# Kernel tuning notes

Hardware: AMD Instinct MI355X
Metric: run time of the kernel (lower is better)

The kernel has to match this reference:

```python
import jax, jax.numpy as jnp
import numpy as np

DIM = 512
NUM_HEADS = 8


def setup_inputs() -> dict:
    key = jax.random.key(0)
    ks = jax.random.split(key, 9)
    B, C, H, W = 8, DIM, 32, 32
    s = 1.0 / np.sqrt(DIM)  # conv-style init scale
    return {
        "x": jax.random.normal(ks[0], (B, C, H, W), jnp.float32),
        "Wq": jax.random.normal(ks[1], (DIM, DIM), jnp.float32) * s,
        "bq": jnp.zeros((DIM,), jnp.float32),
        "Wk": jax.random.normal(ks[2], (DIM, DIM), jnp.float32) * s,
        "bk": jnp.zeros((DIM,), jnp.float32),
        "Wv": jax.random.normal(ks[3], (DIM, DIM), jnp.float32) * s,
        "bv": jnp.zeros((DIM,), jnp.float32),
        "Wo": jax.random.normal(ks[4], (DIM, DIM), jnp.float32) * s,
        "bo": jnp.zeros((DIM,), jnp.float32),
    }


def _proj(x, W, b):
    # 1x1 conv == per-pixel linear over channels: [out_c, in_c] x [b, in_c, h, w]
    return jnp.einsum('oc,bchw->bohw', W, x) + b[None, :, None, None]


def reference(x, Wq, bq, Wk, bk, Wv, bv, Wo, bo):
    b, c, h, w = x.shape
    g = NUM_HEADS
    dh = c // g  # per-head channels
    q = _proj(x, Wq, bq)
    k = _proj(x, Wk, bk)
    v = _proj(x, Wv, bv)
    # 'b (g c) h w -> (b g) c (h w)'
    def split_heads(t):
        return t.reshape(b, g, dh, h * w).reshape(b * g, dh, h * w)
    q, k, v = split_heads(q), split_heads(k), split_heads(v)
    # note: scale uses full dim (as in the source), not per-head dim
    a = jnp.einsum('bcs,bct->bst', q, k) / jnp.sqrt(jnp.float32(c))
    a = jax.nn.softmax(a, axis=-1)  # dropout is identity at inference
    o = jnp.einsum('bst,bct->bcs', a, v)  # [(b g), dh, s]
    o = o.reshape(b, g * dh, h, w)  # '(b g) c (h w) -> b (g c) h w'
    return x + _proj(o, Wo, bo)
```

## Files before the change

### kernel.cpp

```cpp
#include <hip/hip_runtime.h>

typedef unsigned short u16;
typedef __attribute__((ext_vector_type(8))) short short8;
typedef __attribute__((ext_vector_type(4))) short sh4;
typedef __attribute__((ext_vector_type(2))) int int2v;
typedef __attribute__((ext_vector_type(4))) float floatx4;

__device__ __forceinline__ float b2f(u16 u) {
  unsigned int x = ((unsigned int)u) << 16;
  return __builtin_bit_cast(float, x);
}
__device__ __forceinline__ u16 f2b(float f) {
  unsigned int x = __builtin_bit_cast(unsigned int, f);
  unsigned int r = (x + 0x7FFFu + ((x >> 16) & 1u)) >> 16;
  return (u16)r;
}
__device__ __forceinline__ unsigned int pk2bf(float a, float b) {
  unsigned int ua = __builtin_bit_cast(unsigned int, a) + 0x8000u;
  unsigned int ub = __builtin_bit_cast(unsigned int, b) + 0x8000u;
  return __builtin_amdgcn_perm(ub, ua, 0x07060302u);
}

#if __has_builtin(__builtin_amdgcn_mfma_f32_16x16x16bf16_1k)
#define MFMA16(a, b, c) __builtin_amdgcn_mfma_f32_16x16x16bf16_1k((a), (b), (c), 0, 0, 0)
#define MFMA16_DRAIN()
#else
__device__ __forceinline__ floatx4 mfma16_fb(sh4 a, sh4 b, floatx4 c) {
  asm volatile("s_nop 1\n\tv_mfma_f32_16x16x16_bf16 %0, %1, %2, %0"
               : "+v"(c) : "v"(a), "v"(b));
  return c;
}
#define MFMA16(a, b, c) mfma16_fb((a), (b), (c))
#define MFMA16_DRAIN() asm volatile("s_nop 7\n\ts_nop 7\n\ts_nop 7")
#endif

#if __has_builtin(__builtin_amdgcn_exp2f)
#define EXP2F(x) __builtin_amdgcn_exp2f(x)
#else
#define EXP2F(x) __expf((x) * 0.6931471805599453f)
#endif

#define MFMA32(a, b, c) __builtin_amdgcn_mfma_f32_16x16x32_bf16((a), (b), (c), 0, 0, 0)

#define GLL16(g, l) __builtin_amdgcn_global_load_lds(                         \
    (const __attribute__((address_space(1))) unsigned int*)(g),               \
    (__attribute__((address_space(3))) unsigned int*)(l), 16, 0, 0)

#define SC_LOG2E 0.06375872f

__device__ __forceinline__ int detect_fp32(const u16* __restrict__ x) {
  __shared__ int cnt;
  if (threadIdx.x == 0) cnt = 0;
  __syncthreads();
  int c = 0;
  if (threadIdx.x < 256) {
#pragma unroll
    for (int i = 0; i < 16; ++i) {
      u16 u = x[threadIdx.x * 16 + i];
      if (((u >> 7) & 0xFF) >= 0xC8) c++;
    }
  }
  if (c) atomicAdd(&cnt, c);
  __syncthreads();
  return cnt > 32;
}

__global__ __launch_bounds__(256) void prep(
    const u16* __restrict__ x,
    const u16* w0, const u16* w1, const u16* w2, const u16* w3,
    const u16* c0, const u16* c1, const u16* c2, const u16* c3,
    u16* __restrict__ xT, u16* __restrict__ Wc, u16* __restrict__ bc, int b0) {
  const int fp32 = detect_fp32(x);
  const int tid = threadIdx.x;
  if (blockIdx.y < 8) {
    __shared__ u16 t[64][65];
    const int lb = blockIdx.z, b = b0 + lb;
    const int p0 = blockIdx.x * 64, cc0 = blockIdx.y * 64;
    const int tx = tid & 63, ty = tid >> 6;
    if (fp32) {
      const float* xb = (const float*)x + (long)b * 524288;
#pragma unroll
      for (int i = 0; i < 16; ++i) {
        int c = ty + i * 4;
        t[c][tx] = f2b(xb[(long)(cc0 + c) * 1024 + p0 + tx]);
      }
    } else {
      const u16* xb = x + (long)b * 524288;
#pragma unroll
      for (int i = 0; i < 16; ++i) {
        int c = ty + i * 4;
        t[c][tx] = xb[(long)(cc0 + c) * 1024 + p0 + tx];
      }
    }
    __syncthreads();
    u16* xTb = xT + (long)lb * 524288;
#pragma unroll
    for (int i = 0; i < 16; ++i) {
      int p = ty + i * 4;
      xTb[(long)(p0 + p) * 512 + cc0 + tx] = t[tx][p];
    }
  } else {
    const u16* srcs[8] = {w0, w1, w2, w3, c0, c1, c2, c3};
    const int nthreads = gridDim.z * 16 * 256;
    const int flat = (blockIdx.z * 16 + blockIdx.x) * 256 + tid;
    for (int vi = flat; vi < 131072; vi += nthreads) {
      int w = vi >> 15;
      int off = (vi & 32767) * 8;
      u16* dst = Wc + w * 262144 + off;
      if (fp32) {
        const float* s = (const float*)srcs[w] + off;
        u16 tmp[8];
#pragma unroll
        for (int r = 0; r < 8; ++r) tmp[r] = f2b(s[r]);
        *(int4*)dst = *(const int4*)tmp;
      } else {
        *(int4*)dst = *(const int4*)(srcs[w] + off);
      }
    }
    for (int gi = flat; gi < 2048; gi += nthreads) {
      int t2 = gi >> 9;
      bc[gi] = fp32 ? f2b(((const float*)srcs[4 + t2])[gi & 511]) : srcs[4 + t2][gi & 511];
    }
  }
}

struct GemmLds64 {
  u16 As0[128][32], As1[128][32];
  u16 Bs0[128][32], Bs1[128][32];
};

__device__ __forceinline__ void gemm_core64(const u16* __restrict__ A, int lda,
                                            const u16* __restrict__ B, int ldb,
                                            int m0, int n0, int K,
                                            GemmLds64& lds, floatx4 (&acc)[4][4]) {
  const int tid = threadIdx.x;
  const int wave = tid >> 6, lane = tid & 63;
  const int quad = lane >> 4, l15 = lane & 15;
  const int wm = (wave >> 1) * 64, wn = (wave & 1) * 64;
  const int lrow = lane >> 2, lcol = (lane & 3) * 8;
  for (int k0 = 0; k0 < K; k0 += 64) {
    __syncthreads();
#pragma unroll
    for (int it = 0; it < 2; ++it) {
      const int rbase = wave * 32 + it * 16;
      const u16* Ar = A + (long)(m0 + rbase + lrow) * lda + k0 + lcol;
      GLL16(Ar, &lds.As0[rbase][0]);
      GLL16(Ar + 32, &lds.As1[rbase][0]);
      const u16* Br = B + (long)(n0 + rbase + lrow) * ldb + k0 + lcol;
      GLL16(Br, &lds.Bs0[rbase][0]);
      GLL16(Br + 32, &lds.Bs1[rbase][0]);
    }
    __syncthreads();
    short8 af[4], bf[4];
#pragma unroll
    for (int i = 0; i < 4; ++i)
      af[i] = *(const short8*)&lds.As0[wm + i * 16 + l15][quad * 8];
#pragma unroll
    for (int j = 0; j < 4; ++j)
      bf[j] = *(const short8*)&lds.Bs0[wn + j * 16 + l15][quad * 8];
#pragma unroll
    for (int i = 0; i < 4; ++i)
#pragma unroll
      for (int j = 0; j < 4; ++j)
        acc[i][j] = MFMA32(af[i], bf[j], acc[i][j]);
#pragma unroll
    for (int i = 0; i < 4; ++i)
      af[i] = *(const short8*)&lds.As1[wm + i * 16 + l15][quad * 8];
#pragma unroll
    for (int j = 0; j < 4; ++j)
      bf[j] = *(const short8*)&lds.Bs1[wn + j * 16 + l15][quad * 8];
#pragma unroll
    for (int i = 0; i < 4; ++i)
#pragma unroll
      for (int j = 0; j < 4; ++j)
        acc[i][j] = MFMA32(af[i], bf[j], acc[i][j]);
  }
}

__global__ __launch_bounds__(256) void gemm_qkv(
    const u16* __restrict__ xT, const u16* __restrict__ Wc,
    const u16* __restrict__ bc, u16* __restrict__ Qt, u16* __restrict__ Kt,
    u16* __restrict__ Vv) {
  __shared__ GemmLds64 lds;
  const long bz = blockIdx.x;
  const u16* xb = xT + bz * 524288;
  const int bx = blockIdx.y;
  const int qk = bx < 64;
  const int t = qk ? bx : bx - 64;
  const int m0 = (t >> 3) * 128, n0 = (t & 7) * 128;
  const u16* A = qk ? xb : (Wc + 524288);
  const u16* B = qk ? Wc : xb;
  floatx4 acc[4][4] = {};
  gemm_core64(A, 512, B, 512, m0, n0, 512, lds, acc);
  const int lane = threadIdx.x & 63, wave = threadIdx.x >> 6;
  const int quad = lane >> 4, l15 = lane & 15;
  const int wm = (wave >> 1) * 64, wn = (wave & 1) * 64;
  if (qk) {
    u16* Qz = Qt + bz * 524288;
    u16* Kz = Kt + bz * 524288;
#pragma unroll
    for (int i = 0; i < 4; ++i)
#pragma unroll
      for (int j = 0; j < 4; ++j)
#pragma unroll
        for (int r = 0; r < 4; ++r) {
          int gm = m0 + wm + i * 16 + quad * 4 + r;
          int gn = n0 + wn + j * 16 + l15;
          float v = acc[i][j][r] + b2f(bc[gn]);
          if (gn < 512) Qz[(long)gm * 512 + gn] = f2b(v * SC_LOG2E);
          else Kz[(long)gm * 512 + gn - 512] = f2b(v);
        }
  } else {
    u16* Vz = Vv + bz * 524288;
    const u16* bv = bc + 1024;
#pragma unroll
    for (int i = 0; i < 4; ++i)
#pragma unroll
      for (int j = 0; j < 4; ++j)
#pragma unroll
        for (int r = 0; r < 4; ++r) {
          int gm = m0 + wm + i * 16 + quad * 4 + r;
          int gn = n0 + wn + j * 16 + l15;
          float v = acc[i][j][r] + b2f(bv[gm]);
          Vz[(long)gm * 1024 + gn] = f2b(v);
        }
  }
}

struct OutLds64 {
  u16 As0[128][32], As1[128][32];
  u16 Bs0[64][32], Bs1[64][32];
};

__global__ __launch_bounds__(256) void gemm_out(
    const u16* __restrict__ Wo, const u16* __restrict__ bo,
    const u16* __restrict__ Ow, const u16* __restrict__ xraw,
    u16* __restrict__ out) {
  const int fp32 = detect_fp32(xraw);
  __shared__ OutLds64 lds;
  const long bz = blockIdx.x;
  const u16* B = Ow + bz * 524288;
  const int m0 = blockIdx.z * 128, n0 = blockIdx.y * 64;
  const int tid = threadIdx.x;
  const int wave = tid >> 6, lane = tid & 63;
  const int quad = lane >> 4, l15 = lane & 15;
  const int lrow = lane >> 2, lcol = (lane & 3) * 8;

  floatx4 acc[2][4] = {};

  for (int k0 = 0; k0 < 512; k0 += 64) {
    __syncthreads();
    {
      const int ra = wave * 32;
      const u16* A0 = Wo + (long)(m0 + ra + lrow) * 512 + k0 + lcol;
      const u16* A1 = Wo + (long)(m0 + ra + 16 + lrow) * 512 + k0 + lcol;
      GLL16(A0, &lds.As0[ra][0]);
      GLL16(A0 + 32, &lds.As1[ra][0]);
      GLL16(A1, &lds.As0[ra + 16][0]);
      GLL16(A1 + 32, &lds.As1[ra + 16][0]);
      const u16* Br = B + (long)(n0 + wave * 16 + lrow) * 512 + k0 + lcol;
      GLL16(Br, &lds.Bs0[wave * 16][0]);
      GLL16(Br + 32, &lds.Bs1[wave * 16][0]);
    }
    __syncthreads();
#pragma unroll
    for (int i = 0; i < 2; ++i) {
      short8 af = *(const short8*)&lds.As0[wave * 32 + i * 16 + l15][quad * 8];
#pragma unroll
      for (int j = 0; j < 4; ++j) {
        short8 bf = *(const short8*)&lds.Bs0[j * 16 + l15][quad * 8];
        acc[i][j] = MFMA32(af, bf, acc[i][j]);
      }
    }
#pragma unroll
    for (int i = 0; i < 2; ++i) {
      short8 af = *(const short8*)&lds.As1[wave * 32 + i * 16 + l15][quad * 8];
#pragma unroll
      for (int j = 0; j < 4; ++j) {
        short8 bf = *(const short8*)&lds.Bs1[j * 16 + l15][quad * 8];
        acc[i][j] = MFMA32(af, bf, acc[i][j]);
      }
    }
  }

#pragma unroll
  for (int i = 0; i < 2; ++i)
#pragma unroll
    for (int j = 0; j < 4; ++j)
#pragma unroll
      for (int r = 0; r < 4; ++r) {
        int gm = m0 + wave * 32 + i * 16 + quad * 4 + r;
        int gn = n0 + j * 16 + l15;
        float v = acc[i][j][r] + b2f(bo[gm]);
        long idx = bz * 524288 + (long)gm * 1024 + gn;
        if (fp32) {
          v += ((const float*)xraw)[idx];
          ((float*)out)[idx] = v;
        } else {
          v += b2f(xraw[idx]);
          out[idx] = f2b(v);
        }
      }
}

#define AP 72
__global__ __launch_bounds__(256, 2) void attn(
    const u16* __restrict__ Qt, const u16* __restrict__ Kt,
    const u16* __restrict__ V, u16* __restrict__ O) {
  __shared__ alignas(16) u16 Ks[2][64][AP];
  __shared__ alignas(16) u16 Vs[2][64][AP];
  const int bg = blockIdx.x;
  const int lb = bg >> 3, head = bg & 7;
  const int s0 = blockIdx.y * 128;
  const int tid = threadIdx.x;
  const int wave = tid >> 6, lane = tid & 63;
  const int quad = lane >> 4, l15 = lane & 15;

  const u16* Qb = Qt + (long)lb * 524288 + head * 64;
  const u16* Kb = Kt + (long)lb * 524288 + head * 64;
  const u16* Vb = V + (long)(lb * 512 + head * 64) * 1024;
  u16* Ob = O + (long)lb * 524288 + head * 64;

  short8 bq[2][2];
#pragma unroll
  for (int qb = 0; qb < 2; ++qb)
#pragma unroll
    for (int kk = 0; kk < 2; ++kk)
      bq[qb][kk] = *(const short8*)&Qb[(long)(s0 + wave * 32 + qb * 16 + l15) * 512 +
                                       kk * 32 + quad * 8];

  const int r0 = tid >> 3, o0 = (tid & 7) * 8;
  int4 kreg0, kreg1, vreg0, vreg1;
  kreg0 = *(const int4*)&Kb[(long)r0 * 512 + o0];
  kreg1 = *(const int4*)&Kb[(long)(r0 + 32) * 512 + o0];
  vreg0 = *(const int4*)&Vb[(long)r0 * 1024 + o0];
  vreg1 = *(const int4*)&Vb[(long)(r0 + 32) * 1024 + o0];
  *(int4*)&Ks[0][r0][o0] = kreg0;
  *(int4*)&Ks[0][r0 + 32][o0] = kreg1;
  *(int4*)&Vs[0][r0][o0] = vreg0;
  *(int4*)&Vs[0][r0 + 32][o0] = vreg1;

  floatx4 acc[2][4] = {};
  floatx4 accl[2] = {};
  const sh4 ones = {(short)0x3F80, (short)0x3F80, (short)0x3F80, (short)0x3F80};

  for (int it16 = 0; it16 < 16; ++it16) {
    const int buf = it16 & 1;
    const int t0n = (it16 + 1) * 64;
    if (it16 < 15) {
      kreg0 = *(const int4*)&Kb[(long)(t0n + r0) * 512 + o0];
      kreg1 = *(const int4*)&Kb[(long)(t0n + r0 + 32) * 512 + o0];
      vreg0 = *(const int4*)&Vb[(long)r0 * 1024 + t0n + o0];
      vreg1 = *(const int4*)&Vb[(long)(r0 + 32) * 1024 + t0n + o0];
    }
    __syncthreads();

    floatx4 p[2][4] = {};
#pragma unroll
    for (int kk = 0; kk < 2; ++kk) {
      short8 ak[4];
#pragma unroll
      for (int mi = 0; mi < 4; ++mi)
        ak[mi] = *(const short8*)&Ks[buf][mi * 16 + l15][kk * 32 + quad * 8];
#pragma unroll
      for (int qb = 0; qb < 2; ++qb)
#pragma unroll
        for (int mi = 0; mi < 4; ++mi)
          p[qb][mi] = MFMA32(ak[mi], bq[qb][kk], p[qb][mi]);
    }

    sh4 pk[2][4];
#pragma unroll
    for (int qb = 0; qb < 2; ++qb)
#pragma unroll
      for (int mi = 0; mi < 4; ++mi) {
        float e0 = EXP2F(p[qb][mi][0]);
        float e1 = EXP2F(p[qb][mi][1]);
        float e2 = EXP2F(p[qb][mi][2]);
        float e3 = EXP2F(p[qb][mi][3]);
        int2v w;
        w.x = (int)pk2bf(e0, e1);
        w.y = (int)pk2bf(e2, e3);
        pk[qb][mi] = __builtin_bit_cast(sh4, w);
      }

#pragma unroll
    for (int qb = 0; qb < 2; ++qb)
#pragma unroll
      for (int mi = 0; mi < 4; ++mi) accl[qb] = MFMA16(ones, pk[qb][mi], accl[qb]);

#pragma unroll
    for (int mi = 0; mi < 4; ++mi) {
      sh4 av[4];
#pragma unroll
      for (int ci = 0; ci < 4; ++ci)
        av[ci] = *(const sh4*)&Vs[buf][ci * 16 + l15][mi * 16 + quad * 4];
#pragma unroll
      for (int qb = 0; qb < 2; ++qb)
#pragma unroll
        for (int ci = 0; ci < 4; ++ci)
          acc[qb][ci] = MFMA16(av[ci], pk[qb][mi], acc[qb][ci]);
    }

    if (it16 < 15) {
      const int nb = 1 - buf;
      *(int4*)&Ks[nb][r0][o0] = kreg0;
      *(int4*)&Ks[nb][r0 + 32][o0] = kreg1;
      *(int4*)&Vs[nb][r0][o0] = vreg0;
      *(int4*)&Vs[nb][r0 + 32][o0] = vreg1;
    }
  }
  MFMA16_DRAIN();

  const float inv0 = 1.0f / accl[0][0];
  const float inv1 = 1.0f / accl[1][0];

  u16 (*Os)[AP] = (u16(*)[AP]) & Ks[0][0][0];
  __syncthreads();
#pragma unroll
  for (int qb = 0; qb < 2; ++qb) {
    const float inv = qb ? inv1 : inv0;
#pragma unroll
    for (int ci = 0; ci < 4; ++ci) {
      int2v w;
      w.x = (int)pk2bf(acc[qb][ci][0] * inv, acc[qb][ci][1] * inv);
      w.y = (int)pk2bf(acc[qb][ci][2] * inv, acc[qb][ci][3] * inv);
      *(int2v*)&Os[wave * 32 + qb * 16 + l15][ci * 16 + quad * 4] = w;
    }
  }
  __syncthreads();
  {
    const int srow = tid >> 1, cb = (tid & 1) * 32;
#pragma unroll
    for (int c = 0; c < 32; c += 8)
      *(int4*)&Ob[(long)(s0 + srow) * 512 + cb + c] = *(const int4*)&Os[srow][cb + c];
  }
}

extern "C" void kernel_launch(void* const* d_in, const int* in_sizes, int n_in,
                              void* d_out, int out_size, void* d_ws, size_t ws_size,
                              hipStream_t stream) {
  const u16* x  = (const u16*)d_in[0];
  const u16* Wq = (const u16*)d_in[1];
  const u16* bq = (const u16*)d_in[2];
  const u16* Wk = (const u16*)d_in[3];
  const u16* bk = (const u16*)d_in[4];
  const u16* Wv = (const u16*)d_in[5];
  const u16* bv = (const u16*)d_in[6];
  const u16* Wo = (const u16*)d_in[7];
  const u16* bo = (const u16*)d_in[8];
  u16* out = (u16*)d_out;
  u16* ws = (u16*)d_ws;

  const size_t PLAN_A_BYTES = 27267072;

  if (ws_size >= PLAN_A_BYTES) {
    u16* xT = ws;
    u16* Kt = ws + 4194304;
    u16* Vv = ws + 8388608;
    u16* Wc = ws + 12582912;
    u16* bc = ws + 13631488;
    u16* Qt = out;
    u16* Ow = xT;

    prep<<<dim3(16, 9, 8), 256, 0, stream>>>(x, Wq, Wk, Wv, Wo,
                                             bq, bk, bv, bo, xT, Wc, bc, 0);
    gemm_qkv<<<dim3(8, 96), 256, 0, stream>>>(xT, Wc, bc, Qt, Kt, Vv);
    attn<<<dim3(64, 8), 256, 0, stream>>>(Qt, Kt, Vv, Ow);
    gemm_out<<<dim3(8, 16, 4), 256, 0, stream>>>(Wc + 786432, bc + 1536, Ow, x, out);
  } else {
    u16* Ow = ws;
    u16* Kt = ws + 4194304;
    u16* Vv = ws + 6291456;
    u16* Wc = ws + 8388608;
    u16* bc = ws + 9437184;
    u16* Qt = out;

    for (int phase = 0; phase < 2; ++phase) {
      const int b0 = phase * 4;
      u16* xT = Ow + (long)phase * 2097152;
      prep<<<dim3(16, 9, 4), 256, 0, stream>>>(x, Wq, Wk, Wv, Wo,
                                               bq, bk, bv, bo, xT, Wc, bc, b0);
      gemm_qkv<<<dim3(4, 96), 256, 0, stream>>>(xT, Wc, bc, Qt, Kt, Vv);
      attn<<<dim3(32, 8), 256, 0, stream>>>(Qt, Kt, Vv, Ow + (long)b0 * 524288);
    }
    gemm_out<<<dim3(8, 16, 4), 256, 0, stream>>>(Wc + 786432, bc + 1536, Ow, x, out);
  }
}
```

Baseline: 161.1 us.

## Fuse input transpose and weight conversion into QKV GEMM, drop prep kernel

Removes the separate prep kernel that transposed x to bf16 and converted the weights. The QKV GEMM now reads x (fp32 or bf16) directly, converts and transposes it while staging into LDS, and converts the weights on the fly. gemm_out converts Wo on the fly in the same way. This saves one launch and a full round trip of x through the workspace. The cost is an fp32 staging path that uses scalar LDS stores with bank conflicts and recomputes conversions in every tile, instead of async global-to-LDS loads.

```diff
diff --git a/kernel.cpp b/kernel.cpp
--- a/kernel.cpp
+++ b/kernel.cpp
@@ -65,90 +65,118 @@
   return cnt > 32;
 }
 
-__global__ __launch_bounds__(256) void prep(
-    const u16* __restrict__ x,
-    const u16* w0, const u16* w1, const u16* w2, const u16* w3,
-    const u16* c0, const u16* c1, const u16* c2, const u16* c3,
-    u16* __restrict__ xT, u16* __restrict__ Wc, u16* __restrict__ bc, int b0) {
-  const int fp32 = detect_fp32(x);
-  const int tid = threadIdx.x;
-  if (blockIdx.y < 8) {
-    __shared__ u16 t[64][65];
-    const int lb = blockIdx.z, b = b0 + lb;
-    const int p0 = blockIdx.x * 64, cc0 = blockIdx.y * 64;
-    const int tx = tid & 63, ty = tid >> 6;
-    if (fp32) {
-      const float* xb = (const float*)x + (long)b * 524288;
-#pragma unroll
-      for (int i = 0; i < 16; ++i) {
-        int c = ty + i * 4;
-        t[c][tx] = f2b(xb[(long)(cc0 + c) * 1024 + p0 + tx]);
-      }
-    } else {
-      const u16* xb = x + (long)b * 524288;
-#pragma unroll
-      for (int i = 0; i < 16; ++i) {
-        int c = ty + i * 4;
-        t[c][tx] = xb[(long)(cc0 + c) * 1024 + p0 + tx];
-      }
-    }
-    __syncthreads();
-    u16* xTb = xT + (long)lb * 524288;
-#pragma unroll
-    for (int i = 0; i < 16; ++i) {
-      int p = ty + i * 4;
-      xTb[(long)(p0 + p) * 512 + cc0 + tx] = t[tx][p];
-    }
-  } else {
-    const u16* srcs[8] = {w0, w1, w2, w3, c0, c1, c2, c3};
-    const int nthreads = gridDim.z * 16 * 256;
-    const int flat = (blockIdx.z * 16 + blockIdx.x) * 256 + tid;
-    for (int vi = flat; vi < 131072; vi += nthreads) {
-      int w = vi >> 15;
-      int off = (vi & 32767) * 8;
-      u16* dst = Wc + w * 262144 + off;
-      if (fp32) {
-        const float* s = (const float*)srcs[w] + off;
-        u16 tmp[8];
-#pragma unroll
-        for (int r = 0; r < 8; ++r) tmp[r] = f2b(s[r]);
-        *(int4*)dst = *(const int4*)tmp;
-      } else {
-        *(int4*)dst = *(const int4*)(srcs[w] + off);
-      }
-    }
-    for (int gi = flat; gi < 2048; gi += nthreads) {
-      int t2 = gi >> 9;
-      bc[gi] = fp32 ? f2b(((const float*)srcs[4 + t2])[gi & 511]) : srcs[4 + t2][gi & 511];
-    }
-  }
+__device__ __forceinline__ float bload(const u16* p, long i, int fp32) {
+  return fp32 ? ((const float*)p)[i] : b2f(p[i]);
 }
 
 struct GemmLds64 {
   u16 As0[128][32], As1[128][32];
   u16 Bs0[128][32], Bs1[128][32];
 };
-
-__device__ __forceinline__ void gemm_core64(const u16* __restrict__ A, int lda,
-                                            const u16* __restrict__ B, int ldb,
-                                            int m0, int n0, int K,
-                                            GemmLds64& lds, floatx4 (&acc)[4][4]) {
+struct OutLds64 {
+  u16 As0[128][32], As1[128][32];
+  u16 Bs0[64][32], Bs1[64][32];
+};
+#define AP 72
+struct AttnLds {
+  alignas(16) u16 Ks[2][64][AP];
+  alignas(16) u16 Vs[2][64][AP];
+};
+
+__device__ __forceinline__ void stage_xT(const u16* __restrict__ x, int b,
+                                         int fp32, int row0, int k0,
+                                         u16 (*__restrict__ S0)[32],
+                                         u16 (*__restrict__ S1)[32]) {
+  const int tid = threadIdx.x;
+  const int cl = tid & 63, pc = tid >> 6;
+  u16(*__restrict__ S)[32] = (cl < 32) ? S0 : S1;
+  const int c31 = cl & 31;
+  if (fp32) {
+    const float* src = (const float*)x + (long)b * 524288 +
+                       (long)(k0 + cl) * 1024 + row0 + pc * 32;
+#pragma unroll
+    for (int q = 0; q < 4; ++q) {
+      float4 f0 = *(const float4*)(src + q * 8);
+      float4 f1 = *(const float4*)(src + q * 8 + 4);
+      u16 tmp[8] = {f2b(f0.x), f2b(f0.y), f2b(f0.z), f2b(f0.w),
+                    f2b(f1.x), f2b(f1.y), f2b(f1.z), f2b(f1.w)};
+#pragma unroll
+      for (int e = 0; e < 8; ++e) S[pc * 32 + q * 8 + e][c31] = tmp[e];
+    }
+  } else {
+    const u16* src = x + (long)b * 524288 + (long)(k0 + cl) * 1024 + row0 + pc * 32;
+#pragma unroll
+    for (int q = 0; q < 4; ++q) {
+      int4 v = *(const int4*)(src + q * 8);
+      const u16* t = (const u16*)&v;
+#pragma unroll
+      for (int e = 0; e < 8; ++e) S[pc * 32 + q * 8 + e][c31] = t[e];
+    }
+  }
+}
+
+__device__ __forceinline__ void stage_w(const u16* __restrict__ W, int fp32,
+                                        int row0, int ld, int k0,
+                                        u16 (*__restrict__ S0)[32],
+                                        u16 (*__restrict__ S1)[32], int rbase_w) {
+  const int lane = threadIdx.x & 63;
+  const int lrow = lane >> 2, lcol = (lane & 3) * 8;
+  if (!fp32) {
+#pragma unroll
+    for (int it = 0; it < 2; ++it) {
+      const int rb = rbase_w + it * 16;
+      const u16* Wr = W + (long)(row0 + rb + lrow) * ld + k0 + lcol;
+      GLL16(Wr, &S0[rb][0]);
+      GLL16(Wr + 32, &S1[rb][0]);
+    }
+  } else {
+#pragma unroll
+    for (int it = 0; it < 2; ++it) {
+      const int rb = rbase_w + it * 16;
+      const float* Wr = (const float*)W + (long)(row0 + rb + lrow) * ld + k0 + lcol;
+      u16 a[8], b[8];
+#pragma unroll
+      for (int e = 0; e < 8; ++e) {
+        a[e] = f2b(Wr[e]);
+        b[e] = f2b(Wr[32 + e]);
+      }
+      *(int4*)&S0[rb + lrow][lcol] = *(const int4*)a;
+      *(int4*)&S1[rb + lrow][lcol] = *(const int4*)b;
+    }
+  }
+}
+
+__global__ __launch_bounds__(256) void gemm_qkvT(
+    const u16* __restrict__ x, const u16* __restrict__ Wq,
+    const u16* __restrict__ Wk, const u16* __restrict__ Wv,
+    const u16* __restrict__ bq, const u16* __restrict__ bk,
+    const u16* __restrict__ bv, u16* Qt, u16* __restrict__ Kt,
+    u16* __restrict__ Vv, int b0) {
+  const int fp32 = detect_fp32(x);
+  __shared__ GemmLds64 lds;
+  const long bz = blockIdx.x;
+  const int b = b0 + (int)bz;
+  const int bx = blockIdx.y;
+  const int qk = bx < 64;
+  const int t = qk ? bx : bx - 64;
+  const int m0 = (t >> 3) * 128, n0 = (t & 7) * 128;
+  const u16* Wsel = qk ? (n0 < 512 ? Wq : Wk) : Wv;
+  const int wrow0 = qk ? (n0 & 511) : m0;
+
   const int tid = threadIdx.x;
   const int wave = tid >> 6, lane = tid & 63;
   const int quad = lane >> 4, l15 = lane & 15;
   const int wm = (wave >> 1) * 64, wn = (wave & 1) * 64;
-  const int lrow = lane >> 2, lcol = (lane & 3) * 8;
-  for (int k0 = 0; k0 < K; k0 += 64) {
+
+  floatx4 acc[4][4] = {};
+  for (int k0 = 0; k0 < 512; k0 += 64) {
     __syncthreads();
-#pragma unroll
-    for (int it = 0; it < 2; ++it) {
-      const int rbase = wave * 32 + it * 16;
-      const u16* Ar = A + (long)(m0 + rbase + lrow) * lda + k0 + lcol;
-      GLL16(Ar, &lds.As0[rbase][0]);
-      GLL16(Ar + 32, &lds.As1[rbase][0]);
-      const u16* Br = B + (long)(n0 + rbase + lrow) * ldb + k0 + lcol;
-      GLL16(Br, &lds.Bs0[rbase][0]);
-      GLL16(Br + 32, &lds.Bs1[rbase][0]);
+    if (qk) {
+      stage_xT(x, b, fp32, m0, k0, lds.As0, lds.As1);
+      stage_w(Wsel, fp32, wrow0, 512, k0, lds.Bs0, lds.Bs1, wave * 32);
+    } else {
+      stage_w(Wsel, fp32, wrow0, 512, k0, lds.As0, lds.As1, wave * 32);
+      stage_xT(x, b, fp32, n0, k0, lds.Bs0, lds.Bs1);
     }
     __syncthreads();
     short8 af[4], bf[4];
@@ -175,26 +203,7 @@
       for (int j = 0; j < 4; ++j)
         acc[i][j] = MFMA32(af[i], bf[j], acc[i][j]);
   }
-}
-
-__global__ __launch_bounds__(256) void gemm_qkv(
-    const u16* __restrict__ xT, const u16* __restrict__ Wc,
-    const u16* __restrict__ bc, u16* __restrict__ Qt, u16* __restrict__ Kt,
-    u16* __restrict__ Vv) {
-  __shared__ GemmLds64 lds;
-  const long bz = blockIdx.x;
-  const u16* xb = xT + bz * 524288;
-  const int bx = blockIdx.y;
-  const int qk = bx < 64;
-  const int t = qk ? bx : bx - 64;
-  const int m0 = (t >> 3) * 128, n0 = (t & 7) * 128;
-  const u16* A = qk ? xb : (Wc + 524288);
-  const u16* B = qk ? Wc : xb;
-  floatx4 acc[4][4] = {};
-  gemm_core64(A, 512, B, 512, m0, n0, 512, lds, acc);
-  const int lane = threadIdx.x & 63, wave = threadIdx.x >> 6;
-  const int quad = lane >> 4, l15 = lane & 15;
-  const int wm = (wave >> 1) * 64, wn = (wave & 1) * 64;
+
   if (qk) {
     u16* Qz = Qt + bz * 524288;
     u16* Kz = Kt + bz * 524288;
@@ -206,13 +215,12 @@
         for (int r = 0; r < 4; ++r) {
           int gm = m0 + wm + i * 16 + quad * 4 + r;
           int gn = n0 + wn + j * 16 + l15;
-          float v = acc[i][j][r] + b2f(bc[gn]);
+          float v = acc[i][j][r] + bload(gn < 512 ? bq : bk, gn & 511, fp32);
           if (gn < 512) Qz[(long)gm * 512 + gn] = f2b(v * SC_LOG2E);
           else Kz[(long)gm * 512 + gn - 512] = f2b(v);
         }
   } else {
     u16* Vz = Vv + bz * 524288;
-    const u16* bv = bc + 1024;
 #pragma unroll
     for (int i = 0; i < 4; ++i)
 #pragma unroll
@@ -221,16 +229,143 @@
         for (int r = 0; r < 4; ++r) {
           int gm = m0 + wm + i * 16 + quad * 4 + r;
           int gn = n0 + wn + j * 16 + l15;
-          float v = acc[i][j][r] + b2f(bv[gm]);
+          float v = acc[i][j][r] + bload(bv, gm, fp32);
           Vz[(long)gm * 1024 + gn] = f2b(v);
         }
   }
 }
 
-struct OutLds64 {
-  u16 As0[128][32], As1[128][32];
-  u16 Bs0[64][32], Bs1[64][32];
-};
+__global__ __launch_bounds__(256, 2) void attn(
+    const u16* __restrict__ Qt, const u16* __restrict__ Kt,
+    const u16* __restrict__ V, u16* __restrict__ O) {
+  __shared__ AttnLds L;
+  const int bg = blockIdx.x;
+  const int lb = bg >> 3, head = bg & 7;
+  const int s0 = blockIdx.y * 128;
+  const int tid = threadIdx.x;
+  const int wave = tid >> 6, lane = tid & 63;
+  const int quad = lane >> 4, l15 = lane & 15;
+
+  const u16* Qb = Qt + (long)lb * 524288 + head * 64;
+  const u16* Kb = Kt + (long)lb * 524288 + head * 64;
+  const u16* Vb = V + (long)(lb * 512 + head * 64) * 1024;
+  u16* Ob = O + (long)lb * 524288 + head * 64;
+
+  short8 bq[2][2];
+#pragma unroll
+  for (int qb = 0; qb < 2; ++qb)
+#pragma unroll
+    for (int kk = 0; kk < 2; ++kk)
+      bq[qb][kk] = *(const short8*)&Qb[(long)(s0 + wave * 32 + qb * 16 + l15) * 512 +
+                                       kk * 32 + quad * 8];
+
+  const int r0 = tid >> 3, o0 = (tid & 7) * 8;
+  int4 kreg0, kreg1, vreg0, vreg1;
+  kreg0 = *(const int4*)&Kb[(long)r0 * 512 + o0];
+  kreg1 = *(const int4*)&Kb[(long)(r0 + 32) * 512 + o0];
+  vreg0 = *(const int4*)&Vb[(long)r0 * 1024 + o0];
+  vreg1 = *(const int4*)&Vb[(long)(r0 + 32) * 1024 + o0];
+  *(int4*)&L.Ks[0][r0][o0] = kreg0;
+  *(int4*)&L.Ks[0][r0 + 32][o0] = kreg1;
+  *(int4*)&L.Vs[0][r0][o0] = vreg0;
+  *(int4*)&L.Vs[0][r0 + 32][o0] = vreg1;
+
+  floatx4 acc[2][4] = {};
+  floatx4 accl[2] = {};
+  const sh4 ones = {(short)0x3F80, (short)0x3F80, (short)0x3F80, (short)0x3F80};
+
+  for (int it16 = 0; it16 < 16; ++it16) {
+    const int buf = it16 & 1;
+    const int t0n = (it16 + 1) * 64;
+    if (it16 < 15) {
+      kreg0 = *(const int4*)&Kb[(long)(t0n + r0) * 512 + o0];
+      kreg1 = *(const int4*)&Kb[(long)(t0n + r0 + 32) * 512 + o0];
+      vreg0 = *(const int4*)&Vb[(long)r0 * 1024 + t0n + o0];
+      vreg1 = *(const int4*)&Vb[(long)(r0 + 32) * 1024 + t0n + o0];
+    }
+    __syncthreads();
+
+    floatx4 p[2][4] = {};
+#pragma unroll
+    for (int kk = 0; kk < 2; ++kk) {
+      short8 ak[4];
+#pragma unroll
+      for (int mi = 0; mi < 4; ++mi)
+        ak[mi] = *(const short8*)&L.Ks[buf][mi * 16 + l15][kk * 32 + quad * 8];
+#pragma unroll
+      for (int qb = 0; qb < 2; ++qb)
+#pragma unroll
+        for (int mi = 0; mi < 4; ++mi)
+          p[qb][mi] = MFMA32(ak[mi], bq[qb][kk], p[qb][mi]);
+    }
+
+    sh4 pk[2][4];
+#pragma unroll
+    for (int qb = 0; qb < 2; ++qb)
+#pragma unroll
+      for (int mi = 0; mi < 4; ++mi) {
+        float e0 = EXP2F(p[qb][mi][0]);
+        float e1 = EXP2F(p[qb][mi][1]);
+        float e2 = EXP2F(p[qb][mi][2]);
+        float e3 = EXP2F(p[qb][mi][3]);
+        int2v w;
+        w.x = (int)pk2bf(e0, e1);
+        w.y = (int)pk2bf(e2, e3);
+        pk[qb][mi] = __builtin_bit_cast(sh4, w);
+      }
+
+#pragma unroll
+    for (int qb = 0; qb < 2; ++qb)
+#pragma unroll
+      for (int mi = 0; mi < 4; ++mi) accl[qb] = MFMA16(ones, pk[qb][mi], accl[qb]);
+
+#pragma unroll
+    for (int mi = 0; mi < 4; ++mi) {
+      sh4 av[4];
+#pragma unroll
+      for (int ci = 0; ci < 4; ++ci)
+        av[ci] = *(const sh4*)&L.Vs[buf][ci * 16 + l15][mi * 16 + quad * 4];
+#pragma unroll
+      for (int qb = 0; qb < 2; ++qb)
+#pragma unroll
+        for (int ci = 0; ci < 4; ++ci)
+          acc[qb][ci] = MFMA16(av[ci], pk[qb][mi], acc[qb][ci]);
+    }
+
+    if (it16 < 15) {
+      const int nb = 1 - buf;
+      *(int4*)&L.Ks[nb][r0][o0] = kreg0;
+      *(int4*)&L.Ks[nb][r0 + 32][o0] = kreg1;
+      *(int4*)&L.Vs[nb][r0][o0] = vreg0;
+      *(int4*)&L.Vs[nb][r0 + 32][o0] = vreg1;
+    }
+  }
+  MFMA16_DRAIN();
+
+  const float inv0 = 1.0f / accl[0][0];
+  const float inv1 = 1.0f / accl[1][0];
+
+  u16 (*Os)[AP] = (u16(*)[AP]) & L.Ks[0][0][0];
+  __syncthreads();
+#pragma unroll
+  for (int qb = 0; qb < 2; ++qb) {
+    const float inv = qb ? inv1 : inv0;
+#pragma unroll
+    for (int ci = 0; ci < 4; ++ci) {
+      int2v w;
+      w.x = (int)pk2bf(acc[qb][ci][0] * inv, acc[qb][ci][1] * inv);
+      w.y = (int)pk2bf(acc[qb][ci][2] * inv, acc[qb][ci][3] * inv);
+      *(int2v*)&Os[wave * 32 + qb * 16 + l15][ci * 16 + quad * 4] = w;
+    }
+  }
+  __syncthreads();
+  {
+    const int srow = tid >> 1, cb = (tid & 1) * 32;
+#pragma unroll
+    for (int c = 0; c < 32; c += 8)
+      *(int4*)&Ob[(long)(s0 + srow) * 512 + cb + c] = *(const int4*)&Os[srow][cb + c];
+  }
+}
 
 __global__ __launch_bounds__(256) void gemm_out(
     const u16* __restrict__ Wo, const u16* __restrict__ bo,
@@ -250,14 +385,8 @@
 
   for (int k0 = 0; k0 < 512; k0 += 64) {
     __syncthreads();
+    stage_w(Wo, fp32, m0, 512, k0, lds.As0, lds.As1, wave * 32);
     {
-      const int ra = wave * 32;
-      const u16* A0 = Wo + (long)(m0 + ra + lrow) * 512 + k0 + lcol;
-      const u16* A1 = Wo + (long)(m0 + ra + 16 + lrow) * 512 + k0 + lcol;
-      GLL16(A0, &lds.As0[ra][0]);
-      GLL16(A0 + 32, &lds.As1[ra][0]);
-      GLL16(A1, &lds.As0[ra + 16][0]);
-      GLL16(A1 + 32, &lds.As1[ra + 16][0]);
       const u16* Br = B + (long)(n0 + wave * 16 + lrow) * 512 + k0 + lcol;
       GLL16(Br, &lds.Bs0[wave * 16][0]);
       GLL16(Br + 32, &lds.Bs1[wave * 16][0]);
@@ -291,7 +420,7 @@
       for (int r = 0; r < 4; ++r) {
         int gm = m0 + wave * 32 + i * 16 + quad * 4 + r;
         int gn = n0 + j * 16 + l15;
-        float v = acc[i][j][r] + b2f(bo[gm]);
+        float v = acc[i][j][r] + bload(bo, gm, fp32);
         long idx = bz * 524288 + (long)gm * 1024 + gn;
         if (fp32) {
           v += ((const float*)xraw)[idx];
@@ -301,140 +430,6 @@
           out[idx] = f2b(v);
         }
       }
-}
-
-#define AP 72
-__global__ __launch_bounds__(256, 2) void attn(
-    const u16* __restrict__ Qt, const u16* __restrict__ Kt,
-    const u16* __restrict__ V, u16* __restrict__ O) {
-  __shared__ alignas(16) u16 Ks[2][64][AP];
-  __shared__ alignas(16) u16 Vs[2][64][AP];
-  const int bg = blockIdx.x;
-  const int lb = bg >> 3, head = bg & 7;
-  const int s0 = blockIdx.y * 128;
-  const int tid = threadIdx.x;
-  const int wave = tid >> 6, lane = tid & 63;
-  const int quad = lane >> 4, l15 = lane & 15;
-
-  const u16* Qb = Qt + (long)lb * 524288 + head * 64;
-  const u16* Kb = Kt + (long)lb * 524288 + head * 64;
-  const u16* Vb = V + (long)(lb * 512 + head * 64) * 1024;
-  u16* Ob = O + (long)lb * 524288 + head * 64;
-
-  short8 bq[2][2];
-#pragma unroll
-  for (int qb = 0; qb < 2; ++qb)
-#pragma unroll
-    for (int kk = 0; kk < 2; ++kk)
-      bq[qb][kk] = *(const short8*)&Qb[(long)(s0 + wave * 32 + qb * 16 + l15) * 512 +
-                                       kk * 32 + quad * 8];
-
-  const int r0 = tid >> 3, o0 = (tid & 7) * 8;
-  int4 kreg0, kreg1, vreg0, vreg1;
-  kreg0 = *(const int4*)&Kb[(long)r0 * 512 + o0];
-  kreg1 = *(const int4*)&Kb[(long)(r0 + 32) * 512 + o0];
-  vreg0 = *(const int4*)&Vb[(long)r0 * 1024 + o0];
-  vreg1 = *(const int4*)&Vb[(long)(r0 + 32) * 1024 + o0];
-  *(int4*)&Ks[0][r0][o0] = kreg0;
-  *(int4*)&Ks[0][r0 + 32][o0] = kreg1;
-  *(int4*)&Vs[0][r0][o0] = vreg0;
-  *(int4*)&Vs[0][r0 + 32][o0] = vreg1;
-
-  floatx4 acc[2][4] = {};
-  floatx4 accl[2] = {};
-  const sh4 ones = {(short)0x3F80, (short)0x3F80, (short)0x3F80, (short)0x3F80};
-
-  for (int it16 = 0; it16 < 16; ++it16) {
-    const int buf = it16 & 1;
-    const int t0n = (it16 + 1) * 64;
-    if (it16 < 15) {
-      kreg0 = *(const int4*)&Kb[(long)(t0n + r0) * 512 + o0];
-      kreg1 = *(const int4*)&Kb[(long)(t0n + r0 + 32) * 512 + o0];
-      vreg0 = *(const int4*)&Vb[(long)r0 * 1024 + t0n + o0];
-      vreg1 = *(const int4*)&Vb[(long)(r0 + 32) * 1024 + t0n + o0];
-    }
-    __syncthreads();
-
-    floatx4 p[2][4] = {};
-#pragma unroll
-    for (int kk = 0; kk < 2; ++kk) {
-      short8 ak[4];
-#pragma unroll
-      for (int mi = 0; mi < 4; ++mi)
-        ak[mi] = *(const short8*)&Ks[buf][mi * 16 + l15][kk * 32 + quad * 8];
-#pragma unroll
-      for (int qb = 0; qb < 2; ++qb)
-#pragma unroll
-        for (int mi = 0; mi < 4; ++mi)
-          p[qb][mi] = MFMA32(ak[mi], bq[qb][kk], p[qb][mi]);
-    }
-
-    sh4 pk[2][4];
-#pragma unroll
-    for (int qb = 0; qb < 2; ++qb)
-#pragma unroll
-      for (int mi = 0; mi < 4; ++mi) {
-        float e0 = EXP2F(p[qb][mi][0]);
-        float e1 = EXP2F(p[qb][mi][1]);
-        float e2 = EXP2F(p[qb][mi][2]);
-        float e3 = EXP2F(p[qb][mi][3]);
-        int2v w;
-        w.x = (int)pk2bf(e0, e1);
-        w.y = (int)pk2bf(e2, e3);
-        pk[qb][mi] = __builtin_bit_cast(sh4, w);
-      }
-
-#pragma unroll
-    for (int qb = 0; qb < 2; ++qb)
-#pragma unroll
-      for (int mi = 0; mi < 4; ++mi) accl[qb] = MFMA16(ones, pk[qb][mi], accl[qb]);
-
-#pragma unroll
-    for (int mi = 0; mi < 4; ++mi) {
-      sh4 av[4];
-#pragma unroll
-      for (int ci = 0; ci < 4; ++ci)
-        av[ci] = *(const sh4*)&Vs[buf][ci * 16 + l15][mi * 16 + quad * 4];
-#pragma unroll
-      for (int qb = 0; qb < 2; ++qb)
-#pragma unroll
-        for (int ci = 0; ci < 4; ++ci)
-          acc[qb][ci] = MFMA16(av[ci], pk[qb][mi], acc[qb][ci]);
-    }
-
-    if (it16 < 15) {
-      const int nb = 1 - buf;
-      *(int4*)&Ks[nb][r0][o0] = kreg0;
-      *(int4*)&Ks[nb][r0 + 32][o0] = kreg1;
-      *(int4*)&Vs[nb][r0][o0] = vreg0;
-      *(int4*)&Vs[nb][r0 + 32][o0] = vreg1;
-    }
-  }
-  MFMA16_DRAIN();
-
-  const float inv0 = 1.0f / accl[0][0];
-  const float inv1 = 1.0f / accl[1][0];
-
-  u16 (*Os)[AP] = (u16(*)[AP]) & Ks[0][0][0];
-  __syncthreads();
-#pragma unroll
-  for (int qb = 0; qb < 2; ++qb) {
-    const float inv = qb ? inv1 : inv0;
-#pragma unroll
-    for (int ci = 0; ci < 4; ++ci) {
-      int2v w;
-      w.x = (int)pk2bf(acc[qb][ci][0] * inv, acc[qb][ci][1] * inv);
-      w.y = (int)pk2bf(acc[qb][ci][2] * inv, acc[qb][ci][3] * inv);
-      *(int2v*)&Os[wave * 32 + qb * 16 + l15][ci * 16 + quad * 4] = w;
-    }
-  }
-  __syncthreads();
-  {
-    const int srow = tid >> 1, cb = (tid & 1) * 32;
-#pragma unroll
-    for (int c = 0; c < 32; c += 8)
-      *(int4*)&Ob[(long)(s0 + srow) * 512 + cb + c] = *(const int4*)&Os[srow][cb + c];
-  }
 }
 
 extern "C" void kernel_launch(void* const* d_in, const int* in_sizes, int n_in,
@@ -452,38 +447,30 @@
   u16* out = (u16*)d_out;
   u16* ws = (u16*)d_ws;
 
-  const size_t PLAN_A_BYTES = 27267072;
+  const size_t PLAN_A_BYTES = 25165824;
 
   if (ws_size >= PLAN_A_BYTES) {
-    u16* xT = ws;
-    u16* Kt = ws + 4194304;
-    u16* Vv = ws + 8388608;
-    u16* Wc = ws + 12582912;
-    u16* bc = ws + 13631488;
+    u16* Kt = ws;
+    u16* Vv = ws + 4194304;
+    u16* Ow = ws + 8388608;
     u16* Qt = out;
-    u16* Ow = xT;
-
-    prep<<<dim3(16, 9, 8), 256, 0, stream>>>(x, Wq, Wk, Wv, Wo,
-                                             bq, bk, bv, bo, xT, Wc, bc, 0);
-    gemm_qkv<<<dim3(8, 96), 256, 0, stream>>>(xT, Wc, bc, Qt, Kt, Vv);
+
+    gemm_qkvT<<<dim3(8, 96), 256, 0, stream>>>(x, Wq, Wk, Wv, bq, bk, bv,
+                                               Qt, Kt, Vv, 0);
     attn<<<dim3(64, 8), 256, 0, stream>>>(Qt, Kt, Vv, Ow);
-    gemm_out<<<dim3(8, 16, 4), 256, 0, stream>>>(Wc + 786432, bc + 1536, Ow, x, out);
+    gemm_out<<<dim3(8, 16, 4), 256, 0, stream>>>(Wo, bo, Ow, x, out);
   } else {
     u16* Ow = ws;
     u16* Kt = ws + 4194304;
     u16* Vv = ws + 6291456;
-    u16* Wc = ws + 8388608;
-    u16* bc = ws + 9437184;
     u16* Qt = out;
 
     for (int phase = 0; phase < 2; ++phase) {
       const int b0 = phase * 4;
-      u16* xT = Ow + (long)phase * 2097152;
-      prep<<<dim3(16, 9, 4), 256, 0, stream>>>(x, Wq, Wk, Wv, Wo,
-                                               bq, bk, bv, bo, xT, Wc, bc, b0);
-      gemm_qkv<<<dim3(4, 96), 256, 0, stream>>>(xT, Wc, bc, Qt, Kt, Vv);
+      gemm_qkvT<<<dim3(4, 96), 256, 0, stream>>>(x, Wq, Wk, Wv, bq, bk, bv,
+                                                 Qt, Kt, Vv, b0);
       attn<<<dim3(32, 8), 256, 0, stream>>>(Qt, Kt, Vv, Ow + (long)b0 * 524288);
     }
-    gemm_out<<<dim3(8, 16, 4), 256, 0, stream>>>(Wc + 786432, bc + 1536, Ow, x, out);
-  }
-}
+    gemm_out<<<dim3(8, 16, 4), 256, 0, stream>>>(Wo, bo, Ow, x, out);
+  }
+}
```

Measured after the change: 206.9 us. 28.5% more time.

## Double-buffer LDS tiles in QKV and output GEMMs to overlap loads with MFMA

Applied to the files above, without the earlier changes.

Both projection GEMMs move from a load-sync-compute loop over K-steps of 64 to a two-buffer ping-pong over K-steps of 32. The next tile's global-to-LDS load is issued before the MFMAs on the current buffer, and one barrier per step replaces two. The aim is to hide global load latency behind matrix math. The cost is twice as many loop iterations and barriers, with less compute per step to cover each load.

```diff
diff --git a/kernel.cpp b/kernel.cpp
--- a/kernel.cpp
+++ b/kernel.cpp
@@ -124,56 +124,52 @@
   }
 }
 
-struct GemmLds64 {
-  u16 As0[128][32], As1[128][32];
-  u16 Bs0[128][32], Bs1[128][32];
+struct GemmLdsP {
+  u16 As[2][128][32], Bs[2][128][32];
 };
 
-__device__ __forceinline__ void gemm_core64(const u16* __restrict__ A, int lda,
-                                            const u16* __restrict__ B, int ldb,
-                                            int m0, int n0, int K,
-                                            GemmLds64& lds, floatx4 (&acc)[4][4]) {
+__device__ __forceinline__ void gemm_stage(const u16* __restrict__ A, int lda,
+                                           const u16* __restrict__ B, int ldb,
+                                           int m0, int n0, int k0, int buf,
+                                           GemmLdsP& lds) {
+  const int tid = threadIdx.x;
+  const int wave = tid >> 6, lane = tid & 63;
+  const int lrow = lane >> 2, lcol = (lane & 3) * 8;
+#pragma unroll
+  for (int it = 0; it < 2; ++it) {
+    const int rbase = wave * 32 + it * 16;
+    GLL16(A + (long)(m0 + rbase + lrow) * lda + k0 + lcol, &lds.As[buf][rbase][0]);
+    GLL16(B + (long)(n0 + rbase + lrow) * ldb + k0 + lcol, &lds.Bs[buf][rbase][0]);
+  }
+}
+
+__device__ __forceinline__ void gemm_core_pipe(const u16* __restrict__ A, int lda,
+                                               const u16* __restrict__ B, int ldb,
+                                               int m0, int n0, int K,
+                                               GemmLdsP& lds, floatx4 (&acc)[4][4]) {
   const int tid = threadIdx.x;
   const int wave = tid >> 6, lane = tid & 63;
   const int quad = lane >> 4, l15 = lane & 15;
   const int wm = (wave >> 1) * 64, wn = (wave & 1) * 64;
-  const int lrow = lane >> 2, lcol = (lane & 3) * 8;
-  for (int k0 = 0; k0 < K; k0 += 64) {
-    __syncthreads();
-#pragma unroll
-    for (int it = 0; it < 2; ++it) {
-      const int rbase = wave * 32 + it * 16;
-      const u16* Ar = A + (long)(m0 + rbase + lrow) * lda + k0 + lcol;
-      GLL16(Ar, &lds.As0[rbase][0]);
-      GLL16(Ar + 32, &lds.As1[rbase][0]);
-      const u16* Br = B + (long)(n0 + rbase + lrow) * ldb + k0 + lcol;
-      GLL16(Br, &lds.Bs0[rbase][0]);
-      GLL16(Br + 32, &lds.Bs1[rbase][0]);
-    }
-    __syncthreads();
+
+  gemm_stage(A, lda, B, ldb, m0, n0, 0, 0, lds);
+  __syncthreads();
+  for (int k0 = 0; k0 < K; k0 += 32) {
+    const int buf = (k0 >> 5) & 1;
+    if (k0 + 32 < K) gemm_stage(A, lda, B, ldb, m0, n0, k0 + 32, buf ^ 1, lds);
     short8 af[4], bf[4];
 #pragma unroll
     for (int i = 0; i < 4; ++i)
-      af[i] = *(const short8*)&lds.As0[wm + i * 16 + l15][quad * 8];
+      af[i] = *(const short8*)&lds.As[buf][wm + i * 16 + l15][quad * 8];
 #pragma unroll
     for (int j = 0; j < 4; ++j)
-      bf[j] = *(const short8*)&lds.Bs0[wn + j * 16 + l15][quad * 8];
+      bf[j] = *(const short8*)&lds.Bs[buf][wn + j * 16 + l15][quad * 8];
 #pragma unroll
     for (int i = 0; i < 4; ++i)
 #pragma unroll
       for (int j = 0; j < 4; ++j)
         acc[i][j] = MFMA32(af[i], bf[j], acc[i][j]);
-#pragma unroll
-    for (int i = 0; i < 4; ++i)
-      af[i] = *(const short8*)&lds.As1[wm + i * 16 + l15][quad * 8];
-#pragma unroll
-    for (int j = 0; j < 4; ++j)
-      bf[j] = *(const short8*)&lds.Bs1[wn + j * 16 + l15][quad * 8];
-#pragma unroll
-    for (int i = 0; i < 4; ++i)
-#pragma unroll
-      for (int j = 0; j < 4; ++j)
-        acc[i][j] = MFMA32(af[i], bf[j], acc[i][j]);
+    __syncthreads();
   }
 }
 
@@ -181,7 +177,7 @@
     const u16* __restrict__ xT, const u16* __restrict__ Wc,
     const u16* __restrict__ bc, u16* __restrict__ Qt, u16* __restrict__ Kt,
     u16* __restrict__ Vv) {
-  __shared__ GemmLds64 lds;
+  __shared__ GemmLdsP lds;
   const long bz = blockIdx.x;
   const u16* xb = xT + bz * 524288;
   const int bx = blockIdx.y;
@@ -191,7 +187,7 @@
   const u16* A = qk ? xb : (Wc + 524288);
   const u16* B = qk ? Wc : xb;
   floatx4 acc[4][4] = {};
-  gemm_core64(A, 512, B, 512, m0, n0, 512, lds, acc);
+  gemm_core_pipe(A, 512, B, 512, m0, n0, 512, lds, acc);
   const int lane = threadIdx.x & 63, wave = threadIdx.x >> 6;
   const int quad = lane >> 4, l15 = lane & 15;
   const int wm = (wave >> 1) * 64, wn = (wave & 1) * 64;
@@ -227,9 +223,8 @@
   }
 }
 
-struct OutLds64 {
-  u16 As0[128][32], As1[128][32];
-  u16 Bs0[64][32], Bs1[64][32];
+struct OutLdsP {
+  u16 As[2][128][32], Bs[2][64][32];
 };
 
 __global__ __launch_bounds__(256) void gemm_out(
@@ -237,7 +232,7 @@
     const u16* __restrict__ Ow, const u16* __restrict__ xraw,
     u16* __restrict__ out) {
   const int fp32 = detect_fp32(xraw);
-  __shared__ OutLds64 lds;
+  __shared__ OutLdsP lds;
   const long bz = blockIdx.x;
   const u16* B = Ow + bz * 524288;
   const int m0 = blockIdx.z * 128, n0 = blockIdx.y * 64;
@@ -248,40 +243,34 @@
 
   floatx4 acc[2][4] = {};
 
-  for (int k0 = 0; k0 < 512; k0 += 64) {
+#define OUT_STAGE(buf, k0)                                                    \
+  {                                                                           \
+    const int ra = wave * 32;                                                 \
+    GLL16(Wo + (long)(m0 + ra + lrow) * 512 + (k0) + lcol,                    \
+          &lds.As[buf][ra][0]);                                               \
+    GLL16(Wo + (long)(m0 + ra + 16 + lrow) * 512 + (k0) + lcol,               \
+          &lds.As[buf][ra + 16][0]);                                          \
+    GLL16(B + (long)(n0 + wave * 16 + lrow) * 512 + (k0) + lcol,              \
+          &lds.Bs[buf][wave * 16][0]);                                        \
+  }
+
+  OUT_STAGE(0, 0);
+  __syncthreads();
+  for (int k0 = 0; k0 < 512; k0 += 32) {
+    const int buf = (k0 >> 5) & 1;
+    if (k0 + 32 < 512) OUT_STAGE(buf ^ 1, k0 + 32);
+#pragma unroll
+    for (int i = 0; i < 2; ++i) {
+      short8 af = *(const short8*)&lds.As[buf][wave * 32 + i * 16 + l15][quad * 8];
+#pragma unroll
+      for (int j = 0; j < 4; ++j) {
+        short8 bf = *(const short8*)&lds.Bs[buf][j * 16 + l15][quad * 8];
+        acc[i][j] = MFMA32(af, bf, acc[i][j]);
+      }
+    }
     __syncthreads();
-    {
-      const int ra = wave * 32;
-      const u16* A0 = Wo + (long)(m0 + ra + lrow) * 512 + k0 + lcol;
-      const u16* A1 = Wo + (long)(m0 + ra + 16 + lrow) * 512 + k0 + lcol;
-      GLL16(A0, &lds.As0[ra][0]);
-      GLL16(A0 + 32, &lds.As1[ra][0]);
-      GLL16(A1, &lds.As0[ra + 16][0]);
-      GLL16(A1 + 32, &lds.As1[ra + 16][0]);
-      const u16* Br = B + (long)(n0 + wave * 16 + lrow) * 512 + k0 + lcol;
-      GLL16(Br, &lds.Bs0[wave * 16][0]);
-      GLL16(Br + 32, &lds.Bs1[wave * 16][0]);
-    }
-    __syncthreads();
-#pragma unroll
-    for (int i = 0; i < 2; ++i) {
-      short8 af = *(const short8*)&lds.As0[wave * 32 + i * 16 + l15][quad * 8];
-#pragma unroll
-      for (int j = 0; j < 4; ++j) {
-        short8 bf = *(const short8*)&lds.Bs0[j * 16 + l15][quad * 8];
-        acc[i][j] = MFMA32(af, bf, acc[i][j]);
-      }
-    }
-#pragma unroll
-    for (int i = 0; i < 2; ++i) {
-      short8 af = *(const short8*)&lds.As1[wave * 32 + i * 16 + l15][quad * 8];
-#pragma unroll
-      for (int j = 0; j < 4; ++j) {
-        short8 bf = *(const short8*)&lds.Bs1[j * 16 + l15][quad * 8];
-        acc[i][j] = MFMA32(af, bf, acc[i][j]);
-      }
-    }
-  }
+  }
+#undef OUT_STAGE
 
 #pragma unroll
   for (int i = 0; i < 2; ++i)
```

After: 158.8 us. About the same (-1.4%).
